# Kernel optimization log

Hardware: AMD Instinct MI355X
Metric: run time of the kernel (lower is better)

## Reference

```python
import jax, jax.numpy as jnp
import numpy as np

N_GRAPHS = 1000
P = 300                 # nodes per ring graph
N = N_GRAPHS * P        # 300000 nodes
IN_DIM = 2
HID = 128
OUT_DIM = 2


def _ring_edges():
    idx = jnp.arange(N)
    g = idx // P
    pos = idx % P
    nxt = g * P + (pos + 1) % P
    src = jnp.concatenate([idx, nxt])
    dst = jnp.concatenate([nxt, idx])
    return jnp.stack([src, dst]), g


def setup_inputs() -> dict:
    key = jax.random.key(0)
    ks = jax.random.split(key, 11)
    edge_index, batch = _ring_edges()
    x = jax.random.normal(ks[0], (N, IN_DIM), jnp.float32)

    def glorot(k, fan_in, fan_out):
        lim = np.sqrt(6.0 / (fan_in + fan_out)).astype(np.float32)
        return jax.random.uniform(k, (fan_in, fan_out), jnp.float32, -lim, lim)

    return {
        "x": x,
        "edge_index": edge_index,
        "batch": batch,
        "W1": glorot(ks[1], IN_DIM, HID), "b1": jnp.zeros((HID,), jnp.float32),
        "W2": glorot(ks[2], HID, HID),    "b2": jnp.zeros((HID,), jnp.float32),
        "W3": glorot(ks[3], HID, HID),    "b3": jnp.zeros((HID,), jnp.float32),
        "fw1": glorot(ks[4], HID, HID),   "fb1": jnp.zeros((HID,), jnp.float32),
        "fw2": glorot(ks[5], HID, OUT_DIM), "fb2": jnp.zeros((OUT_DIM,), jnp.float32),
    }


def _gcn_conv(x, W, b, src, dst, norm):
    h = x @ W                              # [N, out]
    msg = h[src] * norm[:, None]           # gather + per-edge scale
    agg = jax.ops.segment_sum(msg, dst, num_segments=N)  # scatter-add
    return agg + b


def reference(x, edge_index, batch, W1, b1, W2, b2, W3, b3, fw1, fb1, fw2, fb2):
    loop = jnp.arange(N)
    src = jnp.concatenate([edge_index[0], loop])
    dst = jnp.concatenate([edge_index[1], loop])
    deg = jax.ops.segment_sum(jnp.ones_like(dst, jnp.float32), dst, num_segments=N)
    dis = jax.lax.rsqrt(deg)               # deg >= 1 due to self-loops
    norm = dis[src] * dis[dst]             # per-edge normalization

    h = jax.nn.relu(_gcn_conv(x, W1, b1, src, dst, norm))
    h = jax.nn.relu(_gcn_conv(h, W2, b2, src, dst, norm))
    h = jax.nn.relu(_gcn_conv(h, W3, b3, src, dst, norm))

    # global mean pool per graph
    sums = jax.ops.segment_sum(h, batch, num_segments=N_GRAPHS)
    cnts = jax.ops.segment_sum(jnp.ones((N,), jnp.float32), batch, num_segments=N_GRAPHS)
    pooled = sums / cnts[:, None]

    out = jax.nn.relu(pooled @ fw1 + fb1)
    out = out @ fw2 + fb2
    return out
```

## Files before the change

### kernel.cpp

```cpp
#include <hip/hip_runtime.h>
#include <hip/hip_bf16.h>
#include <stdint.h>

#define P    300
#define HID  128
#define NG   1000
#define NTL  19

typedef __attribute__((ext_vector_type(8))) short bf16x8;
typedef __attribute__((ext_vector_type(4))) float f32x4;

__device__ short g_wsw[2 * HID * HID];

__device__ __forceinline__ short f2bf(float f) {
    union { float f; uint32_t u; } v; v.f = f;
    uint32_t r = v.u + 0x7fffu + ((v.u >> 16) & 1u);
    return (short)(r >> 16);
}
__device__ __forceinline__ float bf2f(short s) {
    union { uint32_t u; float f; } v; v.u = ((uint32_t)(uint16_t)s) << 16;
    return v.f;
}
__device__ __forceinline__ uint32_t pkbf2(float a, float b) {
    union { __hip_bfloat162 h; uint32_t u; } cv;
    cv.h = __float22bfloat162_rn(float2{a, b});
    return cv.u;
}
__device__ __forceinline__ float unpk(int v, int ft) {
    return bf2f((short)(ft ? (((uint32_t)v) >> 16) : (v & 0xffff)));
}

__global__ __launch_bounds__(256) void k_prep(const float* __restrict__ W2,
                                              const float* __restrict__ W3) {
    int b = blockIdx.x;
    const bool perm = (b < 8);
    const float* W = perm ? W2 : W3;
    short* dst = g_wsw + (perm ? 0 : HID * HID);
    int t    = (b & 7) * 256 + threadIdx.x;
    int fkey = t >> 4;
    int kc   = t & 15;
    int fsrc;
    if (perm) {
        int u = fkey >> 5, ft = (fkey >> 4) & 1, l = fkey & 15;
        fsrc = u * 32 + 2 * l + ft;
    } else fsrc = fkey;
    bf16x8 o;
    #pragma unroll
    for (int j = 0; j < 8; ++j)
        o[j] = f2bf(W[(kc * 8 + j) * HID + fsrc]);
    *(bf16x8*)&dst[(fkey * 16 + (kc ^ (fkey & 15))) * 8] = o;
}

__device__ __forceinline__ void avg_epi(const float* G, float vp0, float vn3,
                                        float b, float* o) {
    o[0] = (vp0  + G[0] + G[1]) * (1.0f / 3.0f) + b;
    o[1] = (G[0] + G[1] + G[2]) * (1.0f / 3.0f) + b;
    o[2] = (G[1] + G[2] + G[3]) * (1.0f / 3.0f) + b;
    o[3] = (G[2] + G[3] + vn3 ) * (1.0f / 3.0f) + b;
    #pragma unroll
    for (int i = 0; i < 4; ++i) o[i] = o[i] > 0.f ? o[i] : 0.f;
}

template<int POOL>
__device__ __forceinline__ void run_pass(short* __restrict__ buf,
                                         const short* __restrict__ wbase,
                                         const float* __restrict__ bias,
                                         float* __restrict__ pool, int tid) {
    const int lane = tid & 63, wv = tid >> 6, q = lane >> 4, lm = lane & 15;
    const int ftg0 = wv * 2;
    bf16x8 wf[2][4];
    #pragma unroll
    for (int ft = 0; ft < 2; ++ft) {
        int fkey = (ftg0 + ft) * 16 + lm;
        #pragma unroll
        for (int kk = 0; kk < 4; ++kk)
            wf[ft][kk] = *(const bf16x8*)&wbase[(fkey * 16 + ((4 * kk + q) ^ lm)) * 8];
    }
    float biaf[2];
    #pragma unroll
    for (int ft = 0; ft < 2; ++ft)
        biaf[ft] = POOL ? bias[(ftg0 + ft) * 16 + lm] : bias[wv * 32 + 2 * lm + ft];
    const int sA = (q == 0) ? (48 + lm) : (lane - 16);
    const int sB = (lane + 16) & 63;
    const int fpair = wv * 32 + 2 * lm;
    const int kcs = fpair >> 3, offs = fpair & 7;

    f32x4 Gp[2], Ga[2], Gb[2], Gfirst[2];
    float c15[2] = {0.f, 0.f}, r0G1[2] = {0.f, 0.f};
    float psum[2] = {0.f, 0.f};

    auto mfma_tile = [&](int t, f32x4* G) {
        const short* tb = buf + t * 2048;
        G[0] = f32x4{0.f, 0.f, 0.f, 0.f};
        G[1] = f32x4{0.f, 0.f, 0.f, 0.f};
        #pragma unroll
        for (int kk = 0; kk < 4; ++kk) {
            bf16x8 af = *(const bf16x8*)&tb[(lm * 16 + ((4 * kk + q) ^ lm)) * 8];
            G[0] = __builtin_amdgcn_mfma_f32_16x16x32_bf16(af, wf[0][kk], G[0], 0, 0, 0);
            G[1] = __builtin_amdgcn_mfma_f32_16x16x32_bf16(af, wf[1][kk], G[1], 0, 0, 0);
        }
    };
    auto epi = [&](const f32x4* E, const f32x4* N, int T, bool act) -> int {
        uint32_t uA = pkbf2(E[0][3], E[1][3]);
        uint32_t uB = pkbf2(E[0][0], E[1][0]);
        uint32_t uC = pkbf2(N[0][0], N[1][0]);
        int vA = __shfl((int)uA, sA, 64);
        int vB = __shfl((int)uB, sB, 64);
        int vC = __shfl((int)uC, lm, 64);
        float o[2][4];
        #pragma unroll
        for (int ft = 0; ft < 2; ++ft) {
            float bpA = unpk(vA, ft), bpB = unpk(vB, ft), bpC = unpk(vC, ft);
            float vp0 = (q == 0) ? c15[ft] : bpA;
            float vn3 = (q == 3) ? bpC : bpB;
            avg_epi((const float*)&E[ft], vp0, vn3, biaf[ft], o[ft]);
            c15[ft] = bpA;
            if (act && POOL) psum[ft] += o[ft][0] + o[ft][1] + o[ft][2] + o[ft][3];
        }
        if (act && !POOL) {
            #pragma unroll
            for (int i = 0; i < 4; ++i) {
                int node = T * 16 + q * 4 + i;
                *(uint32_t*)&buf[(node * 16 + (kcs ^ (node & 15))) * 8 + offs] =
                    pkbf2(o[0][i], o[1][i]);
            }
        }
        return vC;
    };

    mfma_tile(0, Gp);
    Gfirst[0] = Gp[0]; Gfirst[1] = Gp[1];

    for (int j = 1; j <= 9; ++j) {
        mfma_tile(2 * j - 1, Ga);
        mfma_tile(2 * j, Gb);
        if (!POOL) __syncthreads();
        int vC0 = epi(Gp, Ga, 2 * j - 2, j > 1);
        if (j == 1) { r0G1[0] = unpk(vC0, 0); r0G1[1] = unpk(vC0, 1); }
        epi(Ga, Gb, 2 * j - 1, true);
        Gp[0] = Gb[0]; Gp[1] = Gb[1];
    }

    float o18[2][4], o0[2][4];
    #pragma unroll
    for (int ft = 0; ft < 2; ++ft) {
        float bpA  = __shfl(Gp[ft][3], sA, 64);
        float bpB  = __shfl(Gp[ft][0], sB, 64);
        float g0r0 = __shfl(Gfirst[ft][0], lm, 64);
        float vp0  = (q == 0) ? c15[ft] : bpA;
        float vn3  = (q == 2) ? g0r0 : bpB;
        avg_epi((const float*)&Gp[ft], vp0, vn3, biaf[ft], o18[ft]);
        float bpW  = __shfl(Gp[ft][3], 32 + lm, 64);
        float bpA0 = __shfl(Gfirst[ft][3], sA, 64);
        float bpB0 = __shfl(Gfirst[ft][0], sB, 64);
        float vp00 = (q == 0) ? bpW : bpA0;
        float vn30 = (q == 3) ? r0G1[ft] : bpB0;
        avg_epi((const float*)&Gfirst[ft], vp00, vn30, biaf[ft], o0[ft]);
        if (POOL) {
            if (q < 3) psum[ft] += o18[ft][0] + o18[ft][1] + o18[ft][2] + o18[ft][3];
            psum[ft] += o0[ft][0] + o0[ft][1] + o0[ft][2] + o0[ft][3];
        }
    }
    if (!POOL) {
        #pragma unroll
        for (int i = 0; i < 4; ++i) {
            if (q < 3) {
                int node = 288 + q * 4 + i;
                *(uint32_t*)&buf[(node * 16 + (kcs ^ (node & 15))) * 8 + offs] =
                    pkbf2(o18[0][i], o18[1][i]);
            }
            int n0 = q * 4 + i;
            *(uint32_t*)&buf[(n0 * 16 + (kcs ^ (n0 & 15))) * 8 + offs] =
                pkbf2(o0[0][i], o0[1][i]);
        }
    }

    if (POOL) {
        #pragma unroll
        for (int ft = 0; ft < 2; ++ft) {
            psum[ft] += __shfl_xor(psum[ft], 16, 64);
            psum[ft] += __shfl_xor(psum[ft], 32, 64);
        }
        if (q == 0) {
            pool[ftg0 * 16 + lm]      = psum[0];
            pool[ftg0 * 16 + 16 + lm] = psum[1];
        }
    }
}

__global__ __launch_bounds__(256, 2) void k_graph(
        const float* __restrict__ x,
        const float* __restrict__ W1,  const float* __restrict__ b1,
        const float* __restrict__ b2v, const float* __restrict__ b3v,
        const float* __restrict__ fw1, const float* __restrict__ fb1,
        const float* __restrict__ fw2, const float* __restrict__ fb2,
        float* __restrict__ out) {
    __shared__ __align__(16) short buf[304 * HID];
    __shared__ __align__(16) float scr[640];
    float* xs    = scr;
    float* pool  = scr;
    float* parts = scr + 128;
    float* s1    = scr + 384;

    const int g = blockIdx.x, tid = threadIdx.x;

    if (tid < 150) *(float4*)&xs[tid * 4] = *(const float4*)&x[g * 600 + tid * 4];
    __syncthreads();

    {
        const int kc1 = tid & 15;
        const int n0  = tid >> 4;
        float w1x[8], w1y[8], b1v[8];
        #pragma unroll
        for (int j = 0; j < 8; ++j) {
            w1x[j] = W1[kc1 * 8 + j];
            w1y[j] = W1[HID + kc1 * 8 + j];
            b1v[j] = b1[kc1 * 8 + j];
        }
        #pragma unroll
        for (int it = 0; it < NTL; ++it) {
            int node = it * 16 + n0;
            uint32_t w[4] = {0u, 0u, 0u, 0u};
            if (node < P) {
                int prev = (node == 0)     ? P - 1 : node - 1;
                int next = (node == P - 1) ? 0     : node + 1;
                float2 xp = *(const float2*)&xs[2 * prev];
                float2 xc = *(const float2*)&xs[2 * node];
                float2 xn = *(const float2*)&xs[2 * next];
                float ax = (xp.x + xc.x + xn.x) * (1.f / 3.f);
                float ay = (xp.y + xc.y + xn.y) * (1.f / 3.f);
                #pragma unroll
                for (int jj = 0; jj < 4; ++jj) {
                    float va = ax * w1x[2*jj]   + ay * w1y[2*jj]   + b1v[2*jj];
                    float vb = ax * w1x[2*jj+1] + ay * w1y[2*jj+1] + b1v[2*jj+1];
                    va = va > 0.f ? va : 0.f;
                    vb = vb > 0.f ? vb : 0.f;
                    w[jj] = pkbf2(va, vb);
                }
            }
            *(uint4*)&buf[(node * 16 + (kc1 ^ (node & 15))) * 8] =
                uint4{w[0], w[1], w[2], w[3]};
        }
    }
    __syncthreads();

    run_pass<0>(buf, g_wsw,             b2v, pool, tid);
    __syncthreads();
    run_pass<1>(buf, g_wsw + HID * HID, b3v, pool, tid);
    __syncthreads();

    {
        int f = tid & 127, half = tid >> 7;
        float p = 0.f;
        const float* fw1c = fw1 + f;
        #pragma unroll 4
        for (int k = half * 64; k < half * 64 + 64; ++k)
            p += pool[k] * fw1c[k * 128];
        parts[half * 128 + f] = p;
    }
    __syncthreads();
    if (tid < 128) {
        float o1 = fb1[tid] + (parts[tid] + parts[128 + tid]) * (1.0f / 300.0f);
        s1[tid] = o1 > 0.f ? o1 : 0.f;
    }
    __syncthreads();
    if (tid < 128) {
        int o = tid >> 6, ln = tid & 63;
        float v = s1[ln] * fw2[ln * 2 + o] + s1[ln + 64] * fw2[(ln + 64) * 2 + o];
        #pragma unroll
        for (int off = 1; off <= 32; off <<= 1)
            v += __shfl_xor(v, off, 64);
        if (ln == 0) out[g * 2 + o] = v + fb2[o];
    }
}

extern "C" void kernel_launch(void* const* d_in, const int* in_sizes, int n_in,
                              void* d_out, int out_size, void* d_ws, size_t ws_size,
                              hipStream_t stream) {
    const float* x   = (const float*)d_in[0];
    const float* W1  = (const float*)d_in[3];
    const float* b1  = (const float*)d_in[4];
    const float* W2  = (const float*)d_in[5];
    const float* b2  = (const float*)d_in[6];
    const float* W3  = (const float*)d_in[7];
    const float* b3  = (const float*)d_in[8];
    const float* fw1 = (const float*)d_in[9];
    const float* fb1 = (const float*)d_in[10];
    const float* fw2 = (const float*)d_in[11];
    const float* fb2 = (const float*)d_in[12];
    float* out = (float*)d_out;

    k_prep <<<dim3(16), dim3(256), 0, stream>>>(W2, W3);
    k_graph<<<dim3(NG), dim3(256), 0, stream>>>(x, W1, b1, b2, b3,
                                                fw1, fb1, fw2, fb2, out);
}
```

Measured before the change: 125.3 us.

## Split ring tiles across two wave groups with 512-thread blocks

Doubles the block to 512 threads and gives each half-block (four waves) its own slice of the 19 row tiles of the ring graph. Group 0 walks tiles 9 down to 0 and group 1 walks tiles 10 to 18, with boundary neighbours precomputed so the two slices stitch together. The aim is to halve the serial per-wave chain of MFMA plus epilogue per graph and raise latency hiding. In exchange the in-place update needs extra barriers and more complex boundary handling, pooled sums are kept per group and combined in the final FC stage, and launch bounds change to 512 threads with a minimum of 4.

```diff
diff --git a/kernel.cpp b/kernel.cpp
--- a/kernel.cpp
+++ b/kernel.cpp
@@ -5,7 +5,6 @@
 #define P    300
 #define HID  128
 #define NG   1000
-#define NTL  19
 
 typedef __attribute__((ext_vector_type(8))) short bf16x8;
 typedef __attribute__((ext_vector_type(4))) float f32x4;
@@ -66,7 +65,9 @@
                                          const short* __restrict__ wbase,
                                          const float* __restrict__ bias,
                                          float* __restrict__ pool, int tid) {
-    const int lane = tid & 63, wv = tid >> 6, q = lane >> 4, lm = lane & 15;
+    const int lane = tid & 63, wvall = tid >> 6;
+    const int grp = wvall >> 2, wv = wvall & 3;
+    const int q = lane >> 4, lm = lane & 15;
     const int ftg0 = wv * 2;
     bf16x8 wf[2][4];
     #pragma unroll
@@ -80,13 +81,12 @@
     #pragma unroll
     for (int ft = 0; ft < 2; ++ft)
         biaf[ft] = POOL ? bias[(ftg0 + ft) * 16 + lm] : bias[wv * 32 + 2 * lm + ft];
-    const int sA = (q == 0) ? (48 + lm) : (lane - 16);
-    const int sB = (lane + 16) & 63;
+    const int sA  = (q == 0) ? (48 + lm) : (lane - 16);
+    const int sAb = (lane - 16) & 63;
+    const int sB  = (lane + 16) & 63;
     const int fpair = wv * 32 + 2 * lm;
     const int kcs = fpair >> 3, offs = fpair & 7;
 
-    f32x4 Gp[2], Ga[2], Gb[2], Gfirst[2];
-    float c15[2] = {0.f, 0.f}, r0G1[2] = {0.f, 0.f};
     float psum[2] = {0.f, 0.f};
 
     auto mfma_tile = [&](int t, f32x4* G) {
@@ -100,78 +100,125 @@
             G[1] = __builtin_amdgcn_mfma_f32_16x16x32_bf16(af, wf[1][kk], G[1], 0, 0, 0);
         }
     };
-    auto epi = [&](const f32x4* E, const f32x4* N, int T, bool act) -> int {
-        uint32_t uA = pkbf2(E[0][3], E[1][3]);
-        uint32_t uB = pkbf2(E[0][0], E[1][0]);
-        uint32_t uC = pkbf2(N[0][0], N[1][0]);
-        int vA = __shfl((int)uA, sA, 64);
-        int vB = __shfl((int)uB, sB, 64);
-        int vC = __shfl((int)uC, lm, 64);
-        float o[2][4];
-        #pragma unroll
-        for (int ft = 0; ft < 2; ++ft) {
-            float bpA = unpk(vA, ft), bpB = unpk(vB, ft), bpC = unpk(vC, ft);
-            float vp0 = (q == 0) ? c15[ft] : bpA;
-            float vn3 = (q == 3) ? bpC : bpB;
-            avg_epi((const float*)&E[ft], vp0, vn3, biaf[ft], o[ft]);
-            c15[ft] = bpA;
-            if (act && POOL) psum[ft] += o[ft][0] + o[ft][1] + o[ft][2] + o[ft][3];
-        }
-        if (act && !POOL) {
+    auto store_rows = [&](int T, float (&o)[2][4]) {
+        #pragma unroll
+        for (int i = 0; i < 4; ++i) {
+            int node = T * 16 + q * 4 + i;
+            *(uint32_t*)&buf[(node * 16 + (kcs ^ (node & 15))) * 8 + offs] =
+                pkbf2(o[0][i], o[1][i]);
+        }
+    };
+    auto accum = [&](float (&o)[2][4]) {
+        #pragma unroll
+        for (int ft = 0; ft < 2; ++ft)
+            psum[ft] += o[ft][0] + o[ft][1] + o[ft][2] + o[ft][3];
+    };
+
+    f32x4 Gc[2], Gn[2];
+
+    if (grp == 0) {
+        float c0[2];
+        mfma_tile(10, Gn);
+        if (!POOL) __syncthreads();
+        {
+            int vZ = __shfl((int)pkbf2(Gn[0][0], Gn[1][0]), lm, 64);
+            c0[0] = unpk(vZ, 0); c0[1] = unpk(vZ, 1);
+        }
+        mfma_tile(9, Gc);
+        if (!POOL) __syncthreads();
+        for (int s = 2; s <= 10; ++s) {
+            mfma_tile(10 - s, Gn);
+            if (!POOL) __syncthreads();
+            int T = 11 - s;
+            uint32_t uE3 = pkbf2(Gc[0][3], Gc[1][3]);
+            uint32_t uE0 = pkbf2(Gc[0][0], Gc[1][0]);
+            uint32_t uN3 = pkbf2(Gn[0][3], Gn[1][3]);
+            int vA = __shfl((int)uE3, sAb, 64);
+            int vB = __shfl((int)uE0, sB, 64);
+            int vZ = __shfl((int)uE0, lm, 64);
+            int vP = __shfl((int)uN3, 48 + lm, 64);
+            float o[2][4];
             #pragma unroll
-            for (int i = 0; i < 4; ++i) {
-                int node = T * 16 + q * 4 + i;
-                *(uint32_t*)&buf[(node * 16 + (kcs ^ (node & 15))) * 8 + offs] =
-                    pkbf2(o[0][i], o[1][i]);
-            }
-        }
-        return vC;
-    };
-
-    mfma_tile(0, Gp);
-    Gfirst[0] = Gp[0]; Gfirst[1] = Gp[1];
-
-    for (int j = 1; j <= 9; ++j) {
-        mfma_tile(2 * j - 1, Ga);
-        mfma_tile(2 * j, Gb);
-        if (!POOL) __syncthreads();
-        int vC0 = epi(Gp, Ga, 2 * j - 2, j > 1);
-        if (j == 1) { r0G1[0] = unpk(vC0, 0); r0G1[1] = unpk(vC0, 1); }
-        epi(Ga, Gb, 2 * j - 1, true);
-        Gp[0] = Gb[0]; Gp[1] = Gb[1];
-    }
-
-    float o18[2][4], o0[2][4];
-    #pragma unroll
-    for (int ft = 0; ft < 2; ++ft) {
-        float bpA  = __shfl(Gp[ft][3], sA, 64);
-        float bpB  = __shfl(Gp[ft][0], sB, 64);
-        float g0r0 = __shfl(Gfirst[ft][0], lm, 64);
-        float vp0  = (q == 0) ? c15[ft] : bpA;
-        float vn3  = (q == 2) ? g0r0 : bpB;
-        avg_epi((const float*)&Gp[ft], vp0, vn3, biaf[ft], o18[ft]);
-        float bpW  = __shfl(Gp[ft][3], 32 + lm, 64);
-        float bpA0 = __shfl(Gfirst[ft][3], sA, 64);
-        float bpB0 = __shfl(Gfirst[ft][0], sB, 64);
-        float vp00 = (q == 0) ? bpW : bpA0;
-        float vn30 = (q == 3) ? r0G1[ft] : bpB0;
-        avg_epi((const float*)&Gfirst[ft], vp00, vn30, biaf[ft], o0[ft]);
-        if (POOL) {
-            if (q < 3) psum[ft] += o18[ft][0] + o18[ft][1] + o18[ft][2] + o18[ft][3];
-            psum[ft] += o0[ft][0] + o0[ft][1] + o0[ft][2] + o0[ft][3];
-        }
-    }
-    if (!POOL) {
-        #pragma unroll
-        for (int i = 0; i < 4; ++i) {
+            for (int ft = 0; ft < 2; ++ft) {
+                float vp0 = (q == 0) ? unpk(vP, ft) : unpk(vA, ft);
+                float vn3 = (q == 3) ? c0[ft] : unpk(vB, ft);
+                avg_epi((const float*)&Gc[ft], vp0, vn3, biaf[ft], o[ft]);
+                c0[ft] = unpk(vZ, ft);
+            }
+            if (POOL) accum(o); else store_rows(T, o);
+            Gc[0] = Gn[0]; Gc[1] = Gn[1];
+        }
+        mfma_tile(18, Gn);
+        if (!POOL) __syncthreads();
+        {
+            uint32_t uE3 = pkbf2(Gc[0][3], Gc[1][3]);
+            uint32_t uE0 = pkbf2(Gc[0][0], Gc[1][0]);
+            uint32_t uN3 = pkbf2(Gn[0][3], Gn[1][3]);
+            int vA = __shfl((int)uE3, sAb, 64);
+            int vB = __shfl((int)uE0, sB, 64);
+            int vP = __shfl((int)uN3, 32 + lm, 64);
+            float o[2][4];
+            #pragma unroll
+            for (int ft = 0; ft < 2; ++ft) {
+                float vp0 = (q == 0) ? unpk(vP, ft) : unpk(vA, ft);
+                float vn3 = (q == 3) ? c0[ft] : unpk(vB, ft);
+                avg_epi((const float*)&Gc[ft], vp0, vn3, biaf[ft], o[ft]);
+            }
+            if (POOL) accum(o); else store_rows(0, o);
+        }
+    } else {
+        float c15[2], g0r0[2];
+        mfma_tile(9, Gn);
+        if (!POOL) __syncthreads();
+        {
+            int v = __shfl((int)pkbf2(Gn[0][3], Gn[1][3]), 48 + lm, 64);
+            c15[0] = unpk(v, 0); c15[1] = unpk(v, 1);
+        }
+        mfma_tile(0, Gn);
+        if (!POOL) __syncthreads();
+        g0r0[0] = __shfl(Gn[0][0], lm, 64);
+        g0r0[1] = __shfl(Gn[1][0], lm, 64);
+        mfma_tile(10, Gc);
+        if (!POOL) __syncthreads();
+        for (int s = 3; s <= 10; ++s) {
+            mfma_tile(8 + s, Gn);
+            if (!POOL) __syncthreads();
+            int T = s + 7;
+            uint32_t uE3 = pkbf2(Gc[0][3], Gc[1][3]);
+            uint32_t uE0 = pkbf2(Gc[0][0], Gc[1][0]);
+            uint32_t uN0 = pkbf2(Gn[0][0], Gn[1][0]);
+            int vA = __shfl((int)uE3, sA, 64);
+            int vB = __shfl((int)uE0, sB, 64);
+            int vC = __shfl((int)uN0, lm, 64);
+            float o[2][4];
+            #pragma unroll
+            for (int ft = 0; ft < 2; ++ft) {
+                float bpA = unpk(vA, ft);
+                float vp0 = (q == 0) ? c15[ft] : bpA;
+                float vn3 = (q == 3) ? unpk(vC, ft) : unpk(vB, ft);
+                avg_epi((const float*)&Gc[ft], vp0, vn3, biaf[ft], o[ft]);
+                c15[ft] = bpA;
+            }
+            if (POOL) accum(o); else store_rows(T, o);
+            Gc[0] = Gn[0]; Gc[1] = Gn[1];
+        }
+        if (!POOL) __syncthreads();
+        {
+            uint32_t uE3 = pkbf2(Gc[0][3], Gc[1][3]);
+            uint32_t uE0 = pkbf2(Gc[0][0], Gc[1][0]);
+            int vA = __shfl((int)uE3, sA, 64);
+            int vB = __shfl((int)uE0, sB, 64);
+            float o[2][4];
+            #pragma unroll
+            for (int ft = 0; ft < 2; ++ft) {
+                float bpA = unpk(vA, ft);
+                float vp0 = (q == 0) ? c15[ft] : bpA;
+                float vn3 = (q == 2) ? g0r0[ft] : unpk(vB, ft);
+                avg_epi((const float*)&Gc[ft], vp0, vn3, biaf[ft], o[ft]);
+            }
             if (q < 3) {
-                int node = 288 + q * 4 + i;
-                *(uint32_t*)&buf[(node * 16 + (kcs ^ (node & 15))) * 8 + offs] =
-                    pkbf2(o18[0][i], o18[1][i]);
-            }
-            int n0 = q * 4 + i;
-            *(uint32_t*)&buf[(n0 * 16 + (kcs ^ (n0 & 15))) * 8 + offs] =
-                pkbf2(o0[0][i], o0[1][i]);
+                if (POOL) accum(o); else store_rows(18, o);
+            }
         }
     }
 
@@ -182,13 +229,13 @@
             psum[ft] += __shfl_xor(psum[ft], 32, 64);
         }
         if (q == 0) {
-            pool[ftg0 * 16 + lm]      = psum[0];
-            pool[ftg0 * 16 + 16 + lm] = psum[1];
-        }
-    }
-}
-
-__global__ __launch_bounds__(256, 2) void k_graph(
+            pool[grp * 128 + ftg0 * 16 + lm]      = psum[0];
+            pool[grp * 128 + ftg0 * 16 + 16 + lm] = psum[1];
+        }
+    }
+}
+
+__global__ __launch_bounds__(512, 4) void k_graph(
         const float* __restrict__ x,
         const float* __restrict__ W1,  const float* __restrict__ b1,
         const float* __restrict__ b2v, const float* __restrict__ b3v,
@@ -196,11 +243,11 @@
         const float* __restrict__ fw2, const float* __restrict__ fb2,
         float* __restrict__ out) {
     __shared__ __align__(16) short buf[304 * HID];
-    __shared__ __align__(16) float scr[640];
+    __shared__ __align__(16) float scr[896];
     float* xs    = scr;
-    float* pool  = scr;
-    float* parts = scr + 128;
-    float* s1    = scr + 384;
+    float* poolv = scr;
+    float* parts = scr + 256;
+    float* s1    = scr + 768;
 
     const int g = blockIdx.x, tid = threadIdx.x;
 
@@ -218,49 +265,52 @@
             b1v[j] = b1[kc1 * 8 + j];
         }
         #pragma unroll
-        for (int it = 0; it < NTL; ++it) {
-            int node = it * 16 + n0;
-            uint32_t w[4] = {0u, 0u, 0u, 0u};
-            if (node < P) {
-                int prev = (node == 0)     ? P - 1 : node - 1;
-                int next = (node == P - 1) ? 0     : node + 1;
-                float2 xp = *(const float2*)&xs[2 * prev];
-                float2 xc = *(const float2*)&xs[2 * node];
-                float2 xn = *(const float2*)&xs[2 * next];
-                float ax = (xp.x + xc.x + xn.x) * (1.f / 3.f);
-                float ay = (xp.y + xc.y + xn.y) * (1.f / 3.f);
-                #pragma unroll
-                for (int jj = 0; jj < 4; ++jj) {
-                    float va = ax * w1x[2*jj]   + ay * w1y[2*jj]   + b1v[2*jj];
-                    float vb = ax * w1x[2*jj+1] + ay * w1y[2*jj+1] + b1v[2*jj+1];
-                    va = va > 0.f ? va : 0.f;
-                    vb = vb > 0.f ? vb : 0.f;
-                    w[jj] = pkbf2(va, vb);
+        for (int it = 0; it < 10; ++it) {
+            int node = it * 32 + n0;
+            if (node < 304) {
+                uint32_t w[4] = {0u, 0u, 0u, 0u};
+                if (node < P) {
+                    int prev = (node == 0)     ? P - 1 : node - 1;
+                    int next = (node == P - 1) ? 0     : node + 1;
+                    float2 xp = *(const float2*)&xs[2 * prev];
+                    float2 xc = *(const float2*)&xs[2 * node];
+                    float2 xn = *(const float2*)&xs[2 * next];
+                    float ax = (xp.x + xc.x + xn.x) * (1.f / 3.f);
+                    float ay = (xp.y + xc.y + xn.y) * (1.f / 3.f);
+                    #pragma unroll
+                    for (int jj = 0; jj < 4; ++jj) {
+                        float va = ax * w1x[2*jj]   + ay * w1y[2*jj]   + b1v[2*jj];
+                        float vb = ax * w1x[2*jj+1] + ay * w1y[2*jj+1] + b1v[2*jj+1];
+                        va = va > 0.f ? va : 0.f;
+                        vb = vb > 0.f ? vb : 0.f;
+                        w[jj] = pkbf2(va, vb);
+                    }
                 }
-            }
-            *(uint4*)&buf[(node * 16 + (kc1 ^ (node & 15))) * 8] =
-                uint4{w[0], w[1], w[2], w[3]};
-        }
-    }
-    __syncthreads();
-
-    run_pass<0>(buf, g_wsw,             b2v, pool, tid);
-    __syncthreads();
-    run_pass<1>(buf, g_wsw + HID * HID, b3v, pool, tid);
+                *(uint4*)&buf[(node * 16 + (kc1 ^ (node & 15))) * 8] =
+                    uint4{w[0], w[1], w[2], w[3]};
+            }
+        }
+    }
+    __syncthreads();
+
+    run_pass<0>(buf, g_wsw,             b2v, poolv, tid);
+    __syncthreads();
+    run_pass<1>(buf, g_wsw + HID * HID, b3v, poolv, tid);
     __syncthreads();
 
     {
-        int f = tid & 127, half = tid >> 7;
+        int f = tid & 127, qt = tid >> 7;
         float p = 0.f;
         const float* fw1c = fw1 + f;
         #pragma unroll 4
-        for (int k = half * 64; k < half * 64 + 64; ++k)
-            p += pool[k] * fw1c[k * 128];
-        parts[half * 128 + f] = p;
+        for (int k = qt * 32; k < qt * 32 + 32; ++k)
+            p += (poolv[k] + poolv[128 + k]) * fw1c[k * 128];
+        parts[qt * 128 + f] = p;
     }
     __syncthreads();
     if (tid < 128) {
-        float o1 = fb1[tid] + (parts[tid] + parts[128 + tid]) * (1.0f / 300.0f);
+        float o1 = fb1[tid] + (parts[tid] + parts[128 + tid] + parts[256 + tid]
+                               + parts[384 + tid]) * (1.0f / 300.0f);
         s1[tid] = o1 > 0.f ? o1 : 0.f;
     }
     __syncthreads();
@@ -291,6 +341,6 @@
     float* out = (float*)d_out;
 
     k_prep <<<dim3(16), dim3(256), 0, stream>>>(W2, W3);
-    k_graph<<<dim3(NG), dim3(256), 0, stream>>>(x, W1, b1, b2, b3,
+    k_graph<<<dim3(NG), dim3(512), 0, stream>>>(x, W1, b1, b2, b3,
                                                 fw1, fb1, fw2, fb2, out);
 }
```

Measured after the change: 138.4 us. 10.5% more time.

## Reorder GCN layer tile schedule to cut per-tile barriers to two

Applied to the files above, without the earlier changes.

The fused layer previously computed MFMA tiles in pairs and placed a __syncthreads before each pair's epilogue, which gave nine barriers per layer. Tiles are now computed in two halves: tiles 10-18 and 0 go into registers first, then one barrier, then the remaining tiles are computed in reverse order while the upper-half epilogues overwrite LDS rows. A second barrier comes before the lower-half epilogues. This keeps up to 19 tiles of accumulators live in registers, which raises VGPR pressure and risks spills or lower occupancy under launch_bounds(256,2).

```diff
diff --git a/kernel.cpp b/kernel.cpp
--- a/kernel.cpp
+++ b/kernel.cpp
@@ -85,8 +85,6 @@
     const int fpair = wv * 32 + 2 * lm;
     const int kcs = fpair >> 3, offs = fpair & 7;
 
-    f32x4 Gp[2], Ga[2], Gb[2], Gfirst[2];
-    float c15[2] = {0.f, 0.f}, r0G1[2] = {0.f, 0.f};
     float psum[2] = {0.f, 0.f};
 
     auto mfma_tile = [&](int t, f32x4* G) {
@@ -100,79 +98,102 @@
             G[1] = __builtin_amdgcn_mfma_f32_16x16x32_bf16(af, wf[1][kk], G[1], 0, 0, 0);
         }
     };
-    auto epi = [&](const f32x4* E, const f32x4* N, int T, bool act) -> int {
-        uint32_t uA = pkbf2(E[0][3], E[1][3]);
-        uint32_t uB = pkbf2(E[0][0], E[1][0]);
-        uint32_t uC = pkbf2(N[0][0], N[1][0]);
-        int vA = __shfl((int)uA, sA, 64);
-        int vB = __shfl((int)uB, sB, 64);
-        int vC = __shfl((int)uC, lm, 64);
-        float o[2][4];
+    auto store_rows = [&](int T, float (&o)[2][4]) {
+        #pragma unroll
+        for (int i = 0; i < 4; ++i) {
+            int node = T * 16 + q * 4 + i;
+            *(uint32_t*)&buf[(node * 16 + (kcs ^ (node & 15))) * 8 + offs] =
+                pkbf2(o[0][i], o[1][i]);
+        }
+    };
+    auto accum = [&](float (&o)[2][4]) {
+        #pragma unroll
+        for (int ft = 0; ft < 2; ++ft)
+            psum[ft] += o[ft][0] + o[ft][1] + o[ft][2] + o[ft][3];
+    };
+
+    float c15[2];
+    auto epi_mid = [&](const f32x4 (&E)[2], uint32_t uN0, float (&o)[2][4]) {
+        uint32_t uE3 = pkbf2(E[0][3], E[1][3]);
+        uint32_t uE0 = pkbf2(E[0][0], E[1][0]);
+        int vA = __shfl((int)uE3, sA, 64);
+        int vB = __shfl((int)uE0, sB, 64);
+        int vC = __shfl((int)uN0, lm, 64);
         #pragma unroll
         for (int ft = 0; ft < 2; ++ft) {
-            float bpA = unpk(vA, ft), bpB = unpk(vB, ft), bpC = unpk(vC, ft);
+            float bpA = unpk(vA, ft);
             float vp0 = (q == 0) ? c15[ft] : bpA;
-            float vn3 = (q == 3) ? bpC : bpB;
+            float vn3 = (q == 3) ? unpk(vC, ft) : unpk(vB, ft);
             avg_epi((const float*)&E[ft], vp0, vn3, biaf[ft], o[ft]);
             c15[ft] = bpA;
-            if (act && POOL) psum[ft] += o[ft][0] + o[ft][1] + o[ft][2] + o[ft][3];
-        }
-        if (act && !POOL) {
+        }
+    };
+
+    f32x4 GH[10][2];
+    f32x4 GL[9][2];
+
+    #pragma unroll
+    for (int k = 0; k < 9; ++k) mfma_tile(10 + k, GH[k]);
+    mfma_tile(0, GH[9]);
+    if (!POOL) __syncthreads();
+
+    #pragma unroll
+    for (int i = 0; i < 9; ++i) {
+        mfma_tile(9 - i, GL[i]);
+        if (i == 0) {
+            int v = __shfl((int)pkbf2(GL[0][0][3], GL[0][1][3]), 48 + lm, 64);
+            c15[0] = unpk(v, 0); c15[1] = unpk(v, 1);
+        }
+        if (i < 8) {
+            float o[2][4];
+            uint32_t uN0 = pkbf2(GH[i + 1][0][0], GH[i + 1][1][0]);
+            epi_mid(GH[i], uN0, o);
+            if (POOL) accum(o); else store_rows(10 + i, o);
+        } else {
+            float o18[2][4];
+            uint32_t uE3 = pkbf2(GH[8][0][3], GH[8][1][3]);
+            uint32_t uE0 = pkbf2(GH[8][0][0], GH[8][1][0]);
+            uint32_t uZ0 = pkbf2(GH[9][0][0], GH[9][1][0]);
+            int vA = __shfl((int)uE3, sA, 64);
+            int vB = __shfl((int)uE0, sB, 64);
+            int vZ = __shfl((int)uZ0, lm, 64);
             #pragma unroll
-            for (int i = 0; i < 4; ++i) {
-                int node = T * 16 + q * 4 + i;
-                *(uint32_t*)&buf[(node * 16 + (kcs ^ (node & 15))) * 8 + offs] =
-                    pkbf2(o[0][i], o[1][i]);
+            for (int ft = 0; ft < 2; ++ft) {
+                float bpA = unpk(vA, ft);
+                float vp0 = (q == 0) ? c15[ft] : bpA;
+                float vn3 = (q == 2) ? unpk(vZ, ft) : unpk(vB, ft);
+                avg_epi((const float*)&GH[8][ft], vp0, vn3, biaf[ft], o18[ft]);
             }
-        }
-        return vC;
-    };
-
-    mfma_tile(0, Gp);
-    Gfirst[0] = Gp[0]; Gfirst[1] = Gp[1];
-
-    for (int j = 1; j <= 9; ++j) {
-        mfma_tile(2 * j - 1, Ga);
-        mfma_tile(2 * j, Gb);
-        if (!POOL) __syncthreads();
-        int vC0 = epi(Gp, Ga, 2 * j - 2, j > 1);
-        if (j == 1) { r0G1[0] = unpk(vC0, 0); r0G1[1] = unpk(vC0, 1); }
-        epi(Ga, Gb, 2 * j - 1, true);
-        Gp[0] = Gb[0]; Gp[1] = Gb[1];
-    }
-
-    float o18[2][4], o0[2][4];
-    #pragma unroll
-    for (int ft = 0; ft < 2; ++ft) {
-        float bpA  = __shfl(Gp[ft][3], sA, 64);
-        float bpB  = __shfl(Gp[ft][0], sB, 64);
-        float g0r0 = __shfl(Gfirst[ft][0], lm, 64);
-        float vp0  = (q == 0) ? c15[ft] : bpA;
-        float vn3  = (q == 2) ? g0r0 : bpB;
-        avg_epi((const float*)&Gp[ft], vp0, vn3, biaf[ft], o18[ft]);
-        float bpW  = __shfl(Gp[ft][3], 32 + lm, 64);
-        float bpA0 = __shfl(Gfirst[ft][3], sA, 64);
-        float bpB0 = __shfl(Gfirst[ft][0], sB, 64);
-        float vp00 = (q == 0) ? bpW : bpA0;
-        float vn30 = (q == 3) ? r0G1[ft] : bpB0;
-        avg_epi((const float*)&Gfirst[ft], vp00, vn30, biaf[ft], o0[ft]);
-        if (POOL) {
-            if (q < 3) psum[ft] += o18[ft][0] + o18[ft][1] + o18[ft][2] + o18[ft][3];
-            psum[ft] += o0[ft][0] + o0[ft][1] + o0[ft][2] + o0[ft][3];
-        }
-    }
-    if (!POOL) {
-        #pragma unroll
-        for (int i = 0; i < 4; ++i) {
-            if (q < 3) {
-                int node = 288 + q * 4 + i;
-                *(uint32_t*)&buf[(node * 16 + (kcs ^ (node & 15))) * 8 + offs] =
-                    pkbf2(o18[0][i], o18[1][i]);
+            if (q < 3) { if (POOL) accum(o18); else store_rows(18, o18); }
+            float o0[2][4];
+            uint32_t uF3 = pkbf2(GH[9][0][3], GH[9][1][3]);
+            int vA0 = __shfl((int)uF3, (lane - 16) & 63, 64);
+            int vB0 = __shfl((int)uZ0, sB, 64);
+            int vP  = __shfl((int)uE3, 32 + lm, 64);
+            uint32_t uG1 = pkbf2(GL[8][0][0], GL[8][1][0]);
+            int vN = __shfl((int)uG1, lm, 64);
+            #pragma unroll
+            for (int ft = 0; ft < 2; ++ft) {
+                float vp0 = (q == 0) ? unpk(vP, ft) : unpk(vA0, ft);
+                float vn3 = (q == 3) ? unpk(vN, ft) : unpk(vB0, ft);
+                avg_epi((const float*)&GH[9][ft], vp0, vn3, biaf[ft], o0[ft]);
             }
-            int n0 = q * 4 + i;
-            *(uint32_t*)&buf[(n0 * 16 + (kcs ^ (n0 & 15))) * 8 + offs] =
-                pkbf2(o0[0][i], o0[1][i]);
-        }
+            if (POOL) accum(o0); else store_rows(0, o0);
+        }
+    }
+    if (!POOL) __syncthreads();
+
+    {
+        int v = __shfl((int)pkbf2(GH[9][0][3], GH[9][1][3]), 48 + lm, 64);
+        c15[0] = unpk(v, 0); c15[1] = unpk(v, 1);
+    }
+    #pragma unroll
+    for (int T = 1; T <= 9; ++T) {
+        float o[2][4];
+        uint32_t uN0 = (T < 9) ? pkbf2(GL[8 - T][0][0], GL[8 - T][1][0])
+                               : pkbf2(GH[0][0][0], GH[0][1][0]);
+        epi_mid(GL[9 - T], uN0, o);
+        if (POOL) accum(o); else store_rows(T, o);
     }
 
     if (POOL) {
```

Measured after the change: 123.3 us. Within noise of the previous version (-1.6%).
